# Kernel tuning notes

Hardware: AMD Instinct MI355X
Metric: run time of the kernel (lower is better)

The kernel has to match this reference:

```python
import jax, jax.numpy as jnp
import numpy as np

N = 100000
E = 640000
ND = 128   # node_dim
ED = 128   # edge_dim
HD = 256   # hidden_dim
EPS = 1e-5


def _mlp_ln(x, W1, b1, W2, b2, W3, b3, g, beta):
    h = jax.nn.relu(x @ W1 + b1)
    h = jax.nn.relu(h @ W2 + b2)
    o = h @ W3 + b3
    mu = jnp.mean(o, axis=-1, keepdims=True)
    var = jnp.mean(jnp.square(o - mu), axis=-1, keepdims=True)
    return (o - mu) * jax.lax.rsqrt(var + EPS) * g + beta


def setup_inputs() -> dict:
    key = jax.random.key(0)
    ks = jax.random.split(key, 20)
    s = 0.02
    inp = {
        "node_emb": jax.random.normal(ks[0], (N, ND), jnp.float32),
        "edge_emb": jax.random.normal(ks[1], (E, ED), jnp.float32),
        "src": jax.random.randint(ks[2], (E,), 0, N),
        "dst": jax.random.randint(ks[3], (E,), 0, N),
        "num_nodes": N,
        # edge MLP: in = 2*ND + ED
        "eW1": jax.random.normal(ks[4], (2 * ND + ED, HD), jnp.float32) * s,
        "eb1": jnp.zeros((HD,), jnp.float32),
        "eW2": jax.random.normal(ks[5], (HD, HD), jnp.float32) * s,
        "eb2": jnp.zeros((HD,), jnp.float32),
        "eW3": jax.random.normal(ks[6], (HD, ED), jnp.float32) * s,
        "eb3": jnp.zeros((ED,), jnp.float32),
        "eg": jnp.ones((ED,), jnp.float32),
        "ebeta": jnp.zeros((ED,), jnp.float32),
        # node MLP: in = ND + ED
        "nW1": jax.random.normal(ks[7], (ND + ED, HD), jnp.float32) * s,
        "nb1": jnp.zeros((HD,), jnp.float32),
        "nW2": jax.random.normal(ks[8], (HD, HD), jnp.float32) * s,
        "nb2": jnp.zeros((HD,), jnp.float32),
        "nW3": jax.random.normal(ks[9], (HD, ND), jnp.float32) * s,
        "nb3": jnp.zeros((ND,), jnp.float32),
        "ng": jnp.ones((ND,), jnp.float32),
        "nbeta": jnp.zeros((ND,), jnp.float32),
    }
    return inp


def reference(node_emb, edge_emb, src, dst, num_nodes,
              eW1, eb1, eW2, eb2, eW3, eb3, eg, ebeta,
              nW1, nb1, nW2, nb2, nW3, nb3, ng, nbeta):
    # Edge update: e' = MLP(concat(h_i, h_j, e)) + e
    edge_input = jnp.concatenate([node_emb[src], node_emb[dst], edge_emb], axis=-1)
    edge_emb_new = _mlp_ln(edge_input, eW1, eb1, eW2, eb2, eW3, eb3, eg, ebeta) + edge_emb
    # Mean aggregation over incoming edges per dst node
    agg = jax.ops.segment_sum(edge_emb_new, dst, num_segments=num_nodes)
    count = jax.ops.segment_sum(jnp.ones((dst.shape[0], 1), node_emb.dtype), dst, num_segments=num_nodes)
    agg = agg / jnp.maximum(count, 1.0)
    # Node update: h' = MLP(concat(h, agg)) + h
    node_input = jnp.concatenate([node_emb, agg], axis=-1)
    node_emb_new = _mlp_ln(node_input, nW1, nb1, nW2, nb2, nW3, nb3, ng, nbeta) + node_emb
    return (node_emb_new, edge_emb_new)
```

## Files before the change

### kernel.cpp

```cpp
#include <hip/hip_runtime.h>
#include <hip/hip_bf16.h>

typedef __attribute__((ext_vector_type(8))) short bf16x8;
typedef __attribute__((ext_vector_type(4))) short s16x4;
typedef __attribute__((ext_vector_type(4))) float f32x4;

__device__ __forceinline__ short f2bf(float f) {
  union { __hip_bfloat16 h; short s; } u;
  u.h = __float2bfloat16(f);
  return u.s;
}

__device__ __forceinline__ void gld_lds16(const short* g, short* l) {
  __builtin_amdgcn_global_load_lds((const __attribute__((address_space(1))) unsigned*)g,
                                   (__attribute__((address_space(3))) unsigned*)l,
                                   16, 0, 0);
}

#define BARX(N) asm volatile("s_waitcnt vmcnt(" #N ") lgkmcnt(0)\ns_barrier" ::: "memory")
#define BARLG() asm volatile("s_waitcnt lgkmcnt(0)\ns_barrier" ::: "memory")

template <bool PERM>
__global__ void prep_kernel(const float* __restrict__ W, short* __restrict__ out, int K, int N) {
  int s = blockIdx.x * 256 + threadIdx.x;
  int NF = N >> 4;
  int total = (K >> 5) * NF * 64;
  if (s >= total) return;
  int l = s & 63, kcf = s >> 6;
  int kc = kcf / NF, f = kcf - kc * NF;
  int kg = l >> 4, l16 = l & 15;
  bf16x8 o;
#pragma unroll
  for (int e = 0; e < 8; ++e) {
    int kh = kc * 32 + kg * 8 + e;
    int k = PERM ? ((kh & ~63) | ((kh & 3) << 4) | ((kh >> 2) & 15)) : kh;
    o[e] = f2bf(W[(size_t)k * N + f * 16 + l16]);
  }
  *(bf16x8*)(out + (size_t)s * 8) = o;
}

__global__ void count_kernel(const int* __restrict__ dst, int* __restrict__ cnt, int E) {
  int i = blockIdx.x * 256 + threadIdx.x;
  if (i < E) atomicAdd(&cnt[dst[i]], 1);
}

__global__ __launch_bounds__(1024) void scan_kernel(const int* __restrict__ cnt,
                                                    int* __restrict__ off,
                                                    int* __restrict__ cursor, int N) {
  __shared__ int wsum[16];
  const int t = threadIdx.x;
  const int w = t >> 6, l = t & 63;
  int running = 0;
  for (int base = 0; base < N; base += 1024) {
    int i = base + t;
    int v = (i < N) ? cnt[i] : 0;
    int x = v;
#pragma unroll
    for (int d = 1; d < 64; d <<= 1) { int y = __shfl_up(x, d); if (l >= d) x += y; }
    if (l == 63) wsum[w] = x;
    __syncthreads();
    if (w == 0) {
      int s = (l < 16) ? wsum[l] : 0;
#pragma unroll
      for (int d = 1; d < 16; d <<= 1) { int y = __shfl_up(s, d); if (l >= d) s += y; }
      if (l < 16) wsum[l] = s;
    }
    __syncthreads();
    int total = wsum[15];
    int wo = (w > 0) ? wsum[w - 1] : 0;
    int excl = running + wo + x - v;
    if (i < N) { off[i] = excl; cursor[i] = excl; }
    running += total;
    __syncthreads();
  }
  if (t == 0) off[N] = running;
}

__global__ void scatter_kernel(const int* __restrict__ dst, int* __restrict__ cursor,
                               int* __restrict__ eidx, int E) {
  int e = blockIdx.x * 256 + threadIdx.x;
  if (e < E) {
    int p = atomicAdd(&cursor[dst[e]], 1);
    eidx[p] = e;
  }
}

__global__ void agg_kernel(const float* __restrict__ edge_out, const int* __restrict__ eidx,
                           const int* __restrict__ off, float* __restrict__ agg, int N) {
  int n = blockIdx.x * 4 + (threadIdx.x >> 6);
  if (n >= N) return;
  int l = threadIdx.x & 63;
  int beg = off[n], end = off[n + 1];
  float ax = 0.f, ay = 0.f;
  int i = beg;
  for (; i + 4 <= end; i += 4) {
    int e0 = eidx[i], e1 = eidx[i + 1], e2 = eidx[i + 2], e3 = eidx[i + 3];
    float2 v0 = *(const float2*)(edge_out + (size_t)e0 * 128 + l * 2);
    float2 v1 = *(const float2*)(edge_out + (size_t)e1 * 128 + l * 2);
    float2 v2 = *(const float2*)(edge_out + (size_t)e2 * 128 + l * 2);
    float2 v3 = *(const float2*)(edge_out + (size_t)e3 * 128 + l * 2);
    ax += v0.x + v1.x + v2.x + v3.x;
    ay += v0.y + v1.y + v2.y + v3.y;
  }
  for (; i < end; ++i) {
    int e = eidx[i];
    float2 v = *(const float2*)(edge_out + (size_t)e * 128 + l * 2);
    ax += v.x; ay += v.y;
  }
  float inv = 1.0f / fmaxf((float)(end - beg), 1.0f);
  *(float2*)(agg + (size_t)n * 128 + l * 2) = make_float2(ax * inv, ay * inv);
}

struct F8 { float4 a, b; };

template <bool IS_EDGE>
__launch_bounds__(512, 2)
__global__ void mlp_kernel(const float* __restrict__ node_emb, const float* __restrict__ edge_emb,
                           const int* __restrict__ src, const int* __restrict__ dst,
                           const short* __restrict__ wAll,
                           const float* __restrict__ b1, const float* __restrict__ b2,
                           const float* __restrict__ b3,
                           const float* __restrict__ gam, const float* __restrict__ bet,
                           const float* __restrict__ agg,
                           float* __restrict__ out_base, int M) {
  extern __shared__ short smem[];
  short* BsBase = smem;
  short* AsBase = smem + 24576;
  short* Hs     = smem + 32768;

  const int tid = threadIdx.x;
  const int m0 = blockIdx.x * 128;
  const int w = tid >> 6, lane = tid & 63, l16 = lane & 15, kg = lane >> 4;
  const int wr = w >> 2, wc = w & 3;

  constexpr int NC1 = IS_EDGE ? 12 : 8;

  const int grow = tid >> 2;
  const int gk = tid & 3;
  const int grc = min(m0 + grow, M - 1);
  const int aslot = (grow >> 4) * 64 + gk * 16 + (grow & 15);
  int gsr = 0, gdr = 0;
  if (IS_EDGE) { gsr = src[grc]; gdr = dst[grc]; }

  float b1v[4], b2v[4];
#pragma unroll
  for (int ct = 0; ct < 4; ++ct) {
    int col = wc * 64 + ct * 16 + l16;
    b1v[ct] = b1[col];
    b2v[ct] = b2[col];
  }
  float b3v[8], gv[8], bev[8];
#pragma unroll
  for (int f = 0; f < 8; ++f) {
    int col = f * 16 + l16;
    b3v[f] = b3[col]; gv[f] = gam[col]; bev[f] = bet[col];
  }

  f32x4 acc[16];
#pragma unroll
  for (int i = 0; i < 16; ++i) { f32x4 z = {0.f, 0.f, 0.f, 0.f}; acc[i] = z; }

  auto bsbuf = [&](int v) -> short* { return BsBase + (size_t)(v % 3) * 8192; };
  auto stage1024 = [&](int v) {
    const short* g = wAll + (size_t)v * 8192;
    short* l = bsbuf(v);
    gld_lds16(g + (size_t)tid * 8, l + (size_t)tid * 8);
    gld_lds16(g + (size_t)(512 + tid) * 8, l + (size_t)(512 + tid) * 8);
  };

  auto gatherA = [&](int c) -> F8 {
    const float* q;
    if (IS_EDGE) {
      if (c < 4)      q = node_emb + (size_t)gsr * 128 + c * 32 + gk * 8;
      else if (c < 8) q = node_emb + (size_t)gdr * 128 + (c - 4) * 32 + gk * 8;
      else            q = edge_emb + (size_t)grc * 128 + (c - 8) * 32 + gk * 8;
    } else {
      if (c < 4) q = node_emb + (size_t)grc * 128 + c * 32 + gk * 8;
      else       q = agg + (size_t)grc * 128 + (c - 4) * 32 + gk * 8;
    }
    F8 r;
    r.a = *(const float4*)q;
    r.b = *(const float4*)(q + 4);
    return r;
  };
  auto writeA = [&](const F8& p, int buf) {
    float t[8];
    *(float4*)t = p.a; *(float4*)(t + 4) = p.b;
    bf16x8 o;
#pragma unroll
    for (int e = 0; e < 8; ++e) o[e] = f2bf(t[e]);
    *(bf16x8*)&AsBase[(size_t)buf * 4096 + (size_t)aslot * 8] = o;
  };

  auto mfma16 = [&](bf16x8* a, bf16x8* b) {
#pragma unroll
    for (int rt = 0; rt < 4; ++rt)
#pragma unroll
      for (int ct = 0; ct < 4; ++ct)
        acc[rt * 4 + ct] = __builtin_amdgcn_mfma_f32_16x16x32_bf16(a[rt], b[ct], acc[rt * 4 + ct], 0, 0, 0);
  };

  auto compA = [&](int i) {
    const short* Ap = AsBase + (size_t)(i & 1) * 4096;
    const short* Bp = bsbuf(i);
    bf16x8 a[4], b[4];
#pragma unroll
    for (int rt = 0; rt < 4; ++rt)
      a[rt] = *(const bf16x8*)&Ap[(size_t)((wr * 4 + rt) * 64 + kg * 16 + l16) * 8];
#pragma unroll
    for (int ct = 0; ct < 4; ++ct)
      b[ct] = *(const bf16x8*)&Bp[(size_t)((wc * 4 + ct) * 64 + lane) * 8];
    mfma16(a, b);
  };

  auto computeH = [&](int j, const short* Bp) {
    bf16x8 a[4], b[4];
#pragma unroll
    for (int rt = 0; rt < 4; ++rt) {
      int row = wr * 64 + rt * 16 + l16;
      int ch = (j * 32 + kg * 8) ^ ((row & 7) << 3);
      a[rt] = *(const bf16x8*)&Hs[(size_t)row * 256 + ch];
    }
#pragma unroll
    for (int ct = 0; ct < 4; ++ct)
      b[ct] = *(const bf16x8*)&Bp[(size_t)((wc * 4 + ct) * 64 + lane) * 8];
    mfma16(a, b);
  };

  auto writeH = [&](const float* bv) {
#pragma unroll
    for (int rt = 0; rt < 4; ++rt)
#pragma unroll
      for (int q = 0; q < 4; ++q) {
        int row = wr * 64 + rt * 16 + kg * 4 + q;
        s16x4 v;
#pragma unroll
        for (int ct = 0; ct < 4; ++ct)
          v[ct] = f2bf(fmaxf(acc[rt * 4 + ct][q] + bv[ct], 0.f));
        int ch = (wc * 64 + l16 * 4) ^ ((row & 7) << 3);
        *(s16x4*)&Hs[(size_t)row * 256 + ch] = v;
      }
#pragma unroll
    for (int i = 0; i < 16; ++i) { f32x4 z = {0.f, 0.f, 0.f, 0.f}; acc[i] = z; }
  };

  auto computeL3 = [&](int kk, const short* Bp) {
    int row = w * 16 + l16;
    int ch = (kk * 32 + kg * 8) ^ ((row & 7) << 3);
    bf16x8 a = *(const bf16x8*)&Hs[(size_t)row * 256 + ch];
    const short* Bsub = Bp + (size_t)(kk & 1) * 4096;
#pragma unroll
    for (int f = 0; f < 8; ++f) {
      bf16x8 b = *(const bf16x8*)&Bsub[(size_t)(f * 64 + lane) * 8];
      acc[f] = __builtin_amdgcn_mfma_f32_16x16x32_bf16(a, b, acc[f], 0, 0, 0);
    }
  };

  F8 hold0 = gatherA(0);
  stage1024(0);
  stage1024(1);
  F8 hold = gatherA(1);
  writeA(hold0, 0);
  BARX(4);

#pragma unroll
  for (int i = 0; i < NC1; ++i) {
    stage1024(i + 2);
    F8 gnew = hold;
    if (i + 2 < NC1) gnew = gatherA(i + 2);
    compA(i);
    if (i + 1 < NC1) writeA(hold, (i + 1) & 1);
    if (i + 2 < NC1) { BARX(4); } else { BARX(2); }
    hold = gnew;
  }
  writeH(b1v);
  BARLG();

#pragma unroll
  for (int j = 0; j < 8; ++j) {
    int p = NC1 + j;
    stage1024(p + 2);
    computeH(j, bsbuf(p));
    BARX(2);
  }
  writeH(b2v);
  BARLG();

#pragma unroll
  for (int k = 0; k < 4; ++k) {
    int p = NC1 + 8 + k;
    if (k < 2) stage1024(p + 2);
    computeL3(2 * k, bsbuf(p));
    computeL3(2 * k + 1, bsbuf(p));
    if (k == 0 || k == 1) { BARX(2); }
    else if (k == 2)      { BARX(0); }
  }

#pragma unroll
  for (int q = 0; q < 4; ++q) {
    int rg = m0 + w * 16 + kg * 4 + q;
    float o[8], s1 = 0.f, s2 = 0.f;
#pragma unroll
    for (int f = 0; f < 8; ++f) {
      float x = acc[f][q] + b3v[f];
      o[f] = x; s1 += x; s2 += x * x;
    }
#pragma unroll
    for (int m = 1; m <= 8; m <<= 1) { s1 += __shfl_xor(s1, m); s2 += __shfl_xor(s2, m); }
    float mu = s1 * (1.f / 128.f);
    float var = s2 * (1.f / 128.f) - mu * mu;
    float rs = rsqrtf(var + 1e-5f);
    if (rg < M) {
      const float* resid = (IS_EDGE ? edge_emb : node_emb) + (size_t)rg * 128;
      float* op = out_base + (size_t)rg * 128;
#pragma unroll
      for (int f = 0; f < 8; ++f) {
        int col = f * 16 + l16;
        op[col] = (o[f] - mu) * rs * gv[f] + bev[f] + resid[col];
      }
    }
  }
}

extern "C" void kernel_launch(void* const* d_in, const int* in_sizes, int n_in,
                              void* d_out, int out_size, void* d_ws, size_t ws_size,
                              hipStream_t stream) {
  const float* node_emb = (const float*)d_in[0];
  const float* edge_emb = (const float*)d_in[1];
  const int*   src      = (const int*)d_in[2];
  const int*   dst      = (const int*)d_in[3];
  const float* eW1 = (const float*)d_in[5];
  const float* eb1 = (const float*)d_in[6];
  const float* eW2 = (const float*)d_in[7];
  const float* eb2 = (const float*)d_in[8];
  const float* eW3 = (const float*)d_in[9];
  const float* eb3 = (const float*)d_in[10];
  const float* eg  = (const float*)d_in[11];
  const float* ebt = (const float*)d_in[12];
  const float* nW1 = (const float*)d_in[13];
  const float* nb1 = (const float*)d_in[14];
  const float* nW2 = (const float*)d_in[15];
  const float* nb2 = (const float*)d_in[16];
  const float* nW3 = (const float*)d_in[17];
  const float* nb3 = (const float*)d_in[18];
  const float* ng  = (const float*)d_in[19];
  const float* nbt = (const float*)d_in[20];

  const int Nn = in_sizes[0] / 128;
  const int Ee = in_sizes[2];

  char* ws = (char*)d_ws;
  float* agg  = (float*)ws;  ws += (size_t)Nn * 128 * 4;
  int* cnt_i  = (int*)ws;    ws += (size_t)Nn * 4;
  int* cursor = (int*)ws;    ws += (size_t)Nn * 4;
  int* offv   = (int*)ws;    ws += (size_t)(Nn + 1) * 4;
  int* eidx   = (int*)ws;    ws += (size_t)Ee * 4;
  ws = (char*)(((uintptr_t)ws + 15) & ~(uintptr_t)15);
  short* wp = (short*)ws;
  short* eAll = wp;
  short* nAll = wp + 196608;

  float* out_node = (float*)d_out;
  float* out_edge = out_node + (size_t)Nn * 128;

  hipMemsetAsync(cnt_i, 0, (size_t)Nn * 4, stream);

  prep_kernel<false><<<48, 256, 0, stream>>>(eW1, eAll, 384, 256);
  prep_kernel<true><<<32, 256, 0, stream>>>(eW2, eAll + 98304, 256, 256);
  prep_kernel<true><<<16, 256, 0, stream>>>(eW3, eAll + 163840, 256, 128);
  prep_kernel<false><<<32, 256, 0, stream>>>(nW1, nAll, 256, 256);
  prep_kernel<true><<<32, 256, 0, stream>>>(nW2, nAll + 65536, 256, 256);
  prep_kernel<true><<<16, 256, 0, stream>>>(nW3, nAll + 131072, 256, 128);

  count_kernel<<<(Ee + 255) / 256, 256, 0, stream>>>(dst, cnt_i, Ee);
  scan_kernel<<<1, 1024, 0, stream>>>(cnt_i, offv, cursor, Nn);
  scatter_kernel<<<(Ee + 255) / 256, 256, 0, stream>>>(dst, cursor, eidx, Ee);

  mlp_kernel<true><<<(Ee + 127) / 128, 512, 131072, stream>>>(
      node_emb, edge_emb, src, dst, eAll,
      eb1, eb2, eb3, eg, ebt, agg, out_edge, Ee);

  agg_kernel<<<(Nn + 3) / 4, 256, 0, stream>>>(out_edge, eidx, offv, agg, Nn);

  mlp_kernel<false><<<(Nn + 127) / 128, 512, 131072, stream>>>(
      node_emb, edge_emb, src, dst, nAll,
      nb1, nb2, nb3, ng, nbt, agg, out_node, Nn);
}
```

Before: 751.8 us.

## Pre-convert node embeddings to bf16, stage A tiles via direct LDS loads, parallelize scan

Node embeddings are converted to bf16 once, and the aggregate is stored in bf16. The MLP kernel can then load gathered A-operand tiles straight into LDS with global_load_lds instead of going through registers and converting fp32 in place. The single-block scan is replaced by a three-kernel parallel scan, the LDS footprint is reduced, and the pipeline loops are rolled with explicit 3-buffer staging. Costs are an extra conversion pass over the node embeddings, an extra bf16 rounding of the aggregate, and rolled loops that may schedule less tightly.

```diff
diff --git a/kernel.cpp b/kernel.cpp
--- a/kernel.cpp
+++ b/kernel.cpp
@@ -19,6 +19,19 @@
 
 #define BARX(N) asm volatile("s_waitcnt vmcnt(" #N ") lgkmcnt(0)\ns_barrier" ::: "memory")
 #define BARLG() asm volatile("s_waitcnt lgkmcnt(0)\ns_barrier" ::: "memory")
+
+__global__ void cvt_kernel(const float* __restrict__ in, short* __restrict__ out, long n8) {
+  long i = (long)blockIdx.x * blockDim.x + threadIdx.x;
+  const long stride = (long)gridDim.x * blockDim.x;
+  for (; i < n8; i += stride) {
+    const float* p = in + i * 8;
+    float4 a = *(const float4*)p, b = *(const float4*)(p + 4);
+    bf16x8 o;
+    o[0] = f2bf(a.x); o[1] = f2bf(a.y); o[2] = f2bf(a.z); o[3] = f2bf(a.w);
+    o[4] = f2bf(b.x); o[5] = f2bf(b.y); o[6] = f2bf(b.z); o[7] = f2bf(b.w);
+    *(bf16x8*)(out + i * 8) = o;
+  }
+}
 
 template <bool PERM>
 __global__ void prep_kernel(const float* __restrict__ W, short* __restrict__ out, int K, int N) {
@@ -44,36 +57,60 @@
   if (i < E) atomicAdd(&cnt[dst[i]], 1);
 }
 
-__global__ __launch_bounds__(1024) void scan_kernel(const int* __restrict__ cnt,
-                                                    int* __restrict__ off,
-                                                    int* __restrict__ cursor, int N) {
-  __shared__ int wsum[16];
-  const int t = threadIdx.x;
-  const int w = t >> 6, l = t & 63;
-  int running = 0;
-  for (int base = 0; base < N; base += 1024) {
-    int i = base + t;
-    int v = (i < N) ? cnt[i] : 0;
-    int x = v;
-#pragma unroll
-    for (int d = 1; d < 64; d <<= 1) { int y = __shfl_up(x, d); if (l >= d) x += y; }
-    if (l == 63) wsum[w] = x;
-    __syncthreads();
-    if (w == 0) {
-      int s = (l < 16) ? wsum[l] : 0;
-#pragma unroll
-      for (int d = 1; d < 16; d <<= 1) { int y = __shfl_up(s, d); if (l >= d) s += y; }
-      if (l < 16) wsum[l] = s;
-    }
-    __syncthreads();
-    int total = wsum[15];
-    int wo = (w > 0) ? wsum[w - 1] : 0;
-    int excl = running + wo + x - v;
+__global__ void bsum_kernel(const int* __restrict__ cnt, int* __restrict__ bsum, int N) {
+  __shared__ int wsum[4];
+  int b = blockIdx.x, t = threadIdx.x;
+  int base = b * 2048;
+  int s = 0;
+#pragma unroll
+  for (int j = 0; j < 8; ++j) {
+    int i = base + j * 256 + t;
+    s += (i < N) ? cnt[i] : 0;
+  }
+#pragma unroll
+  for (int m = 1; m < 64; m <<= 1) s += __shfl_xor(s, m);
+  if ((t & 63) == 0) wsum[t >> 6] = s;
+  __syncthreads();
+  if (t == 0) bsum[b] = wsum[0] + wsum[1] + wsum[2] + wsum[3];
+}
+
+__global__ void bscan_kernel(int* __restrict__ bsum, int nb) {
+  int l = threadIdx.x;
+  int v = (l < nb) ? bsum[l] : 0;
+  int x = v;
+#pragma unroll
+  for (int d = 1; d < 64; d <<= 1) { int y = __shfl_up(x, d); if (l >= d) x += y; }
+  if (l < nb) bsum[l] = x - v;
+}
+
+__global__ void offs_kernel(const int* __restrict__ cnt, const int* __restrict__ bsum,
+                            int* __restrict__ off, int* __restrict__ cursor, int N) {
+  __shared__ int wpre[4];
+  int b = blockIdx.x, t = threadIdx.x, w = t >> 6, l = t & 63;
+  int base = b * 2048;
+  int v[8];
+  int s = 0;
+#pragma unroll
+  for (int j = 0; j < 8; ++j) {
+    int i = base + t * 8 + j;
+    v[j] = (i < N) ? cnt[i] : 0;
+    s += v[j];
+  }
+  int x = s;
+#pragma unroll
+  for (int d = 1; d < 64; d <<= 1) { int y = __shfl_up(x, d); if (l >= d) x += y; }
+  if (l == 63) wpre[w] = x;
+  __syncthreads();
+  int wo = 0;
+  for (int k = 0; k < w; ++k) wo += wpre[k];
+  int excl = bsum[b] + wo + x - s;
+#pragma unroll
+  for (int j = 0; j < 8; ++j) {
+    int i = base + t * 8 + j;
     if (i < N) { off[i] = excl; cursor[i] = excl; }
-    running += total;
-    __syncthreads();
-  }
-  if (t == 0) off[N] = running;
+    excl += v[j];
+  }
+  if (b == gridDim.x - 1 && t == 255) off[N] = excl;
 }
 
 __global__ void scatter_kernel(const int* __restrict__ dst, int* __restrict__ cursor,
@@ -86,7 +123,7 @@
 }
 
 __global__ void agg_kernel(const float* __restrict__ edge_out, const int* __restrict__ eidx,
-                           const int* __restrict__ off, float* __restrict__ agg, int N) {
+                           const int* __restrict__ off, short* __restrict__ aggb, int N) {
   int n = blockIdx.x * 4 + (threadIdx.x >> 6);
   if (n >= N) return;
   int l = threadIdx.x & 63;
@@ -108,37 +145,37 @@
     ax += v.x; ay += v.y;
   }
   float inv = 1.0f / fmaxf((float)(end - beg), 1.0f);
-  *(float2*)(agg + (size_t)n * 128 + l * 2) = make_float2(ax * inv, ay * inv);
+  unsigned pk = ((unsigned)(unsigned short)f2bf(ay * inv) << 16) |
+                (unsigned)(unsigned short)f2bf(ax * inv);
+  *(unsigned*)&aggb[(size_t)n * 128 + l * 2] = pk;
 }
 
 struct F8 { float4 a, b; };
 
 template <bool IS_EDGE>
-__launch_bounds__(512, 2)
-__global__ void mlp_kernel(const float* __restrict__ node_emb, const float* __restrict__ edge_emb,
+__launch_bounds__(512)
+__global__ void mlp_kernel(const float* __restrict__ node_emb_f, const float* __restrict__ edge_emb_f,
+                           const short* __restrict__ node_bf, const short* __restrict__ agg_bf,
                            const int* __restrict__ src, const int* __restrict__ dst,
                            const short* __restrict__ wAll,
                            const float* __restrict__ b1, const float* __restrict__ b2,
                            const float* __restrict__ b3,
                            const float* __restrict__ gam, const float* __restrict__ bet,
-                           const float* __restrict__ agg,
                            float* __restrict__ out_base, int M) {
   extern __shared__ short smem[];
-  short* BsBase = smem;
-  short* AsBase = smem + 24576;
-  short* Hs     = smem + 32768;
+  short* Bs = smem;
+  short* Hs = smem + 24576;
 
   const int tid = threadIdx.x;
   const int m0 = blockIdx.x * 128;
   const int w = tid >> 6, lane = tid & 63, l16 = lane & 15, kg = lane >> 4;
   const int wr = w >> 2, wc = w & 3;
 
-  constexpr int NC1 = IS_EDGE ? 12 : 8;
-
-  const int grow = tid >> 2;
-  const int gk = tid & 3;
+  constexpr int NL1 = IS_EDGE ? 12 : 8;
+
+  const int grow = ((tid >> 6) & 7) * 16 + (tid & 15);
+  const int gcq = ((tid >> 4) & 3) * 8;
   const int grc = min(m0 + grow, M - 1);
-  const int aslot = (grow >> 4) * 64 + gk * 16 + (grow & 15);
   int gsr = 0, gdr = 0;
   if (IS_EDGE) { gsr = src[grc]; gdr = dst[grc]; }
 
@@ -160,39 +197,50 @@
 #pragma unroll
   for (int i = 0; i < 16; ++i) { f32x4 z = {0.f, 0.f, 0.f, 0.f}; acc[i] = z; }
 
-  auto bsbuf = [&](int v) -> short* { return BsBase + (size_t)(v % 3) * 8192; };
-  auto stage1024 = [&](int v) {
+  auto stageW = [&](int v) {
     const short* g = wAll + (size_t)v * 8192;
-    short* l = bsbuf(v);
+    short* l = Bs + (size_t)(v % 3) * 8192;
     gld_lds16(g + (size_t)tid * 8, l + (size_t)tid * 8);
-    gld_lds16(g + (size_t)(512 + tid) * 8, l + (size_t)(512 + tid) * 8);
-  };
-
-  auto gatherA = [&](int c) -> F8 {
-    const float* q;
+    gld_lds16(g + (size_t)(tid + 512) * 8, l + (size_t)(tid + 512) * 8);
+  };
+  auto stageAb = [&](int v) {
+    short* dstp = Hs + (size_t)(v % 3) * 4096 + (size_t)tid * 8;
+    int col = v * 32 + gcq;
+    const short* q;
     if (IS_EDGE) {
-      if (c < 4)      q = node_emb + (size_t)gsr * 128 + c * 32 + gk * 8;
-      else if (c < 8) q = node_emb + (size_t)gdr * 128 + (c - 4) * 32 + gk * 8;
-      else            q = edge_emb + (size_t)grc * 128 + (c - 8) * 32 + gk * 8;
+      q = node_bf + (size_t)(col < 128 ? gsr : gdr) * 128 + (col & 127);
     } else {
-      if (c < 4) q = node_emb + (size_t)grc * 128 + c * 32 + gk * 8;
-      else       q = agg + (size_t)grc * 128 + (c - 4) * 32 + gk * 8;
-    }
+      q = (col < 128) ? node_bf + (size_t)grc * 128 + col
+                      : agg_bf + (size_t)grc * 128 + (col - 128);
+    }
+    gld_lds16(q, dstp);
+  };
+  auto loadAf = [&](int v) -> F8 {
+    const float* q = edge_emb_f + (size_t)grc * 128 + (v * 32 + gcq - 256);
     F8 r;
     r.a = *(const float4*)q;
     r.b = *(const float4*)(q + 4);
     return r;
   };
-  auto writeA = [&](const F8& p, int buf) {
+  auto storeAf = [&](int v, const F8& p) {
     float t[8];
     *(float4*)t = p.a; *(float4*)(t + 4) = p.b;
     bf16x8 o;
 #pragma unroll
     for (int e = 0; e < 8; ++e) o[e] = f2bf(t[e]);
-    *(bf16x8*)&AsBase[(size_t)buf * 4096 + (size_t)aslot * 8] = o;
-  };
-
-  auto mfma16 = [&](bf16x8* a, bf16x8* b) {
+    *(bf16x8*)(Hs + (size_t)(v % 3) * 4096 + (size_t)tid * 8) = o;
+  };
+
+  auto compA = [&](int u) {
+    const short* Ap = Hs + (size_t)(u % 3) * 4096;
+    const short* Bp = Bs + (size_t)(u % 3) * 8192;
+    bf16x8 a[4], b[4];
+#pragma unroll
+    for (int rt = 0; rt < 4; ++rt)
+      a[rt] = *(const bf16x8*)&Ap[(size_t)((wr * 4 + rt) * 64 + lane) * 8];
+#pragma unroll
+    for (int ct = 0; ct < 4; ++ct)
+      b[ct] = *(const bf16x8*)&Bp[(size_t)((wc * 4 + ct) * 64 + lane) * 8];
 #pragma unroll
     for (int rt = 0; rt < 4; ++rt)
 #pragma unroll
@@ -200,31 +248,22 @@
         acc[rt * 4 + ct] = __builtin_amdgcn_mfma_f32_16x16x32_bf16(a[rt], b[ct], acc[rt * 4 + ct], 0, 0, 0);
   };
 
-  auto compA = [&](int i) {
-    const short* Ap = AsBase + (size_t)(i & 1) * 4096;
-    const short* Bp = bsbuf(i);
+  auto compH = [&](int kc, const short* Bp) {
     bf16x8 a[4], b[4];
 #pragma unroll
-    for (int rt = 0; rt < 4; ++rt)
-      a[rt] = *(const bf16x8*)&Ap[(size_t)((wr * 4 + rt) * 64 + kg * 16 + l16) * 8];
+    for (int rt = 0; rt < 4; ++rt) {
+      int row = wr * 64 + rt * 16 + l16;
+      int ch = (kc * 32 + kg * 8) ^ ((row & 7) << 3);
+      a[rt] = *(const bf16x8*)&Hs[(size_t)row * 256 + ch];
+    }
 #pragma unroll
     for (int ct = 0; ct < 4; ++ct)
       b[ct] = *(const bf16x8*)&Bp[(size_t)((wc * 4 + ct) * 64 + lane) * 8];
-    mfma16(a, b);
-  };
-
-  auto computeH = [&](int j, const short* Bp) {
-    bf16x8 a[4], b[4];
-#pragma unroll
-    for (int rt = 0; rt < 4; ++rt) {
-      int row = wr * 64 + rt * 16 + l16;
-      int ch = (j * 32 + kg * 8) ^ ((row & 7) << 3);
-      a[rt] = *(const bf16x8*)&Hs[(size_t)row * 256 + ch];
-    }
-#pragma unroll
-    for (int ct = 0; ct < 4; ++ct)
-      b[ct] = *(const bf16x8*)&Bp[(size_t)((wc * 4 + ct) * 64 + lane) * 8];
-    mfma16(a, b);
+#pragma unroll
+    for (int rt = 0; rt < 4; ++rt)
+#pragma unroll
+      for (int ct = 0; ct < 4; ++ct)
+        acc[rt * 4 + ct] = __builtin_amdgcn_mfma_f32_16x16x32_bf16(a[rt], b[ct], acc[rt * 4 + ct], 0, 0, 0);
   };
 
   auto writeH = [&](const float* bv) {
@@ -244,7 +283,7 @@
     for (int i = 0; i < 16; ++i) { f32x4 z = {0.f, 0.f, 0.f, 0.f}; acc[i] = z; }
   };
 
-  auto computeL3 = [&](int kk, const short* Bp) {
+  auto compL3 = [&](int kk, const short* Bp) {
     int row = w * 16 + l16;
     int ch = (kk * 32 + kg * 8) ^ ((row & 7) << 3);
     bf16x8 a = *(const bf16x8*)&Hs[(size_t)row * 256 + ch];
@@ -256,44 +295,71 @@
     }
   };
 
-  F8 hold0 = gatherA(0);
-  stage1024(0);
-  stage1024(1);
-  F8 hold = gatherA(1);
-  writeA(hold0, 0);
-  BARX(4);
-
-#pragma unroll
-  for (int i = 0; i < NC1; ++i) {
-    stage1024(i + 2);
-    F8 gnew = hold;
-    if (i + 2 < NC1) gnew = gatherA(i + 2);
-    compA(i);
-    if (i + 1 < NC1) writeA(hold, (i + 1) & 1);
-    if (i + 2 < NC1) { BARX(4); } else { BARX(2); }
-    hold = gnew;
+  stageW(0);
+  stageAb(0);
+  stageW(1);
+  stageAb(1);
+  BARX(3);
+
+#pragma unroll 1
+  for (int u = 0; u < 6; ++u) {
+    stageW(u + 2);
+    stageAb(u + 2);
+    compA(u);
+    BARX(3);
+  }
+
+  if (IS_EDGE) {
+#pragma unroll 1
+    for (int u = 6; u < 10; ++u) {
+      F8 p = loadAf(u + 2);
+      stageW(u + 2);
+      compA(u);
+      storeAf(u + 2, p);
+      BARX(2);
+    }
+  }
+
+#pragma unroll 1
+  for (int u = NL1 - 2; u < NL1; ++u) {
+    stageW(u + 2);
+    compA(u);
+    BARX(2);
   }
   writeH(b1v);
   BARLG();
 
-#pragma unroll
-  for (int j = 0; j < 8; ++j) {
-    int p = NC1 + j;
-    stage1024(p + 2);
-    computeH(j, bsbuf(p));
+#pragma unroll 1
+  for (int u = NL1; u < NL1 + 8; ++u) {
+    stageW(u + 2);
+    compH(u - NL1, Bs + (size_t)(u % 3) * 8192);
     BARX(2);
   }
   writeH(b2v);
   BARLG();
 
-#pragma unroll
-  for (int k = 0; k < 4; ++k) {
-    int p = NC1 + 8 + k;
-    if (k < 2) stage1024(p + 2);
-    computeL3(2 * k, bsbuf(p));
-    computeL3(2 * k + 1, bsbuf(p));
-    if (k == 0 || k == 1) { BARX(2); }
-    else if (k == 2)      { BARX(0); }
+  {
+    const int us = NL1 + 8;
+#pragma unroll 1
+    for (int k = 0; k < 2; ++k) {
+      int u = us + k;
+      stageW(u + 2);
+      const short* Bp = Bs + (size_t)(u % 3) * 8192;
+      compL3(2 * k, Bp);
+      compL3(2 * k + 1, Bp);
+      BARX(2);
+    }
+    {
+      const short* Bp = Bs + (size_t)((us + 2) % 3) * 8192;
+      compL3(4, Bp);
+      compL3(5, Bp);
+      BARX(0);
+    }
+    {
+      const short* Bp = Bs + (size_t)((us + 3) % 3) * 8192;
+      compL3(6, Bp);
+      compL3(7, Bp);
+    }
   }
 
 #pragma unroll
@@ -311,7 +377,7 @@
     float var = s2 * (1.f / 128.f) - mu * mu;
     float rs = rsqrtf(var + 1e-5f);
     if (rg < M) {
-      const float* resid = (IS_EDGE ? edge_emb : node_emb) + (size_t)rg * 128;
+      const float* resid = (IS_EDGE ? edge_emb_f : node_emb_f) + (size_t)rg * 128;
       float* op = out_base + (size_t)rg * 128;
 #pragma unroll
       for (int f = 0; f < 8; ++f) {
@@ -348,22 +414,26 @@
 
   const int Nn = in_sizes[0] / 128;
   const int Ee = in_sizes[2];
+  const int nb2048 = (Nn + 2047) / 2048;
 
   char* ws = (char*)d_ws;
-  float* agg  = (float*)ws;  ws += (size_t)Nn * 128 * 4;
-  int* cnt_i  = (int*)ws;    ws += (size_t)Nn * 4;
-  int* cursor = (int*)ws;    ws += (size_t)Nn * 4;
-  int* offv   = (int*)ws;    ws += (size_t)(Nn + 1) * 4;
-  int* eidx   = (int*)ws;    ws += (size_t)Ee * 4;
+  short* aggb   = (short*)ws;  ws += (size_t)Nn * 128 * 2;
+  short* nodebf = (short*)ws;  ws += (size_t)Nn * 128 * 2;
+  int* cnt_i  = (int*)ws;      ws += (size_t)Nn * 4;
+  int* cursor = (int*)ws;      ws += (size_t)Nn * 4;
+  int* offv   = (int*)ws;      ws += (size_t)(Nn + 1) * 4;
+  int* eidx   = (int*)ws;      ws += (size_t)Ee * 4;
+  int* bsum   = (int*)ws;      ws += 64 * 4;
   ws = (char*)(((uintptr_t)ws + 15) & ~(uintptr_t)15);
-  short* wp = (short*)ws;
-  short* eAll = wp;
-  short* nAll = wp + 196608;
+  short* eAll = (short*)ws;
+  short* nAll = eAll + 196608;
 
   float* out_node = (float*)d_out;
   float* out_edge = out_node + (size_t)Nn * 128;
 
   hipMemsetAsync(cnt_i, 0, (size_t)Nn * 4, stream);
+
+  cvt_kernel<<<2048, 256, 0, stream>>>(node_emb, nodebf, (long)Nn * 16);
 
   prep_kernel<false><<<48, 256, 0, stream>>>(eW1, eAll, 384, 256);
   prep_kernel<true><<<32, 256, 0, stream>>>(eW2, eAll + 98304, 256, 256);
@@ -373,16 +443,18 @@
   prep_kernel<true><<<16, 256, 0, stream>>>(nW3, nAll + 131072, 256, 128);
 
   count_kernel<<<(Ee + 255) / 256, 256, 0, stream>>>(dst, cnt_i, Ee);
-  scan_kernel<<<1, 1024, 0, stream>>>(cnt_i, offv, cursor, Nn);
+  bsum_kernel<<<nb2048, 256, 0, stream>>>(cnt_i, bsum, Nn);
+  bscan_kernel<<<1, 64, 0, stream>>>(bsum, nb2048);
+  offs_kernel<<<nb2048, 256, 0, stream>>>(cnt_i, bsum, offv, cursor, Nn);
   scatter_kernel<<<(Ee + 255) / 256, 256, 0, stream>>>(dst, cursor, eidx, Ee);
 
-  mlp_kernel<true><<<(Ee + 127) / 128, 512, 131072, stream>>>(
-      node_emb, edge_emb, src, dst, eAll,
-      eb1, eb2, eb3, eg, ebt, agg, out_edge, Ee);
-
-  agg_kernel<<<(Nn + 3) / 4, 256, 0, stream>>>(out_edge, eidx, offv, agg, Nn);
-
-  mlp_kernel<false><<<(Nn + 127) / 128, 512, 131072, stream>>>(
-      node_emb, edge_emb, src, dst, nAll,
-      nb1, nb2, nb3, ng, nbt, agg, out_node, Nn);
-}
+  mlp_kernel<true><<<(Ee + 127) / 128, 512, 114688, stream>>>(
+      node_emb, edge_emb, nodebf, aggb, src, dst, eAll,
+      eb1, eb2, eb3, eg, ebt, out_edge, Ee);
+
+  agg_kernel<<<(Nn + 3) / 4, 256, 0, stream>>>(out_edge, eidx, offv, aggb, Nn);
+
+  mlp_kernel<false><<<(Nn + 127) / 128, 512, 114688, stream>>>(
+      node_emb, edge_emb, nodebf, aggb, src, dst, nAll,
+      nb1, nb2, nb3, ng, nbt, out_node, Nn);
+}
```

Measured after the change: 673.3 us. 1.12x faster.
